# Kernel tuning notes

Measured on AMD Instinct MI355X. Metric: run time of the kernel, lower is better.

## Reference

```python
import jax, jax.numpy as jnp
import numpy as np


def _bilinear_resample(inputs, offsets):
    # inputs: (b, s, s, c); offsets: (b, s, s, 2) -- faithful to tf_batch_map_offsets
    b, h, w, c = inputs.shape
    s = h  # square map assumed by original code (input_size = shape[1])
    n = h * w
    offs = offsets.reshape(b, n, 2)
    gi, gj = jnp.meshgrid(jnp.arange(s, dtype=inputs.dtype),
                          jnp.arange(s, dtype=inputs.dtype), indexing='ij')
    grid = jnp.stack([gi, gj], axis=-1).reshape(1, n, 2)
    coords = jnp.clip(offs + grid, 0.0, float(s - 1))  # (b, n, 2), [i, j]
    lt = jnp.floor(coords).astype(jnp.int32)  # (b, n, 2)
    rb = jnp.ceil(coords).astype(jnp.int32)
    bidx = jnp.arange(b)[:, None]  # (b, 1) broadcasts with (b, n) index maps

    def gather(ci, cj):
        return inputs[bidx, ci, cj]  # (b, n, c)

    vals_lt = gather(lt[..., 0], lt[..., 1])
    vals_rb = gather(rb[..., 0], rb[..., 1])
    vals_lb = gather(rb[..., 0], lt[..., 1])  # [ceil_i, floor_j]
    vals_rt = gather(lt[..., 0], rb[..., 1])  # [floor_i, ceil_j]

    frac = coords - lt.astype(coords.dtype)  # (b, n, 2) fractional offsets
    fy = frac[..., 1:2]  # column fraction (axis 1 of coords)
    fx = frac[..., 0:1]  # row fraction
    vals_t = vals_lt + (vals_rt - vals_lt) * fy
    vals_b = vals_lb + (vals_rb - vals_lb) * fy
    out = vals_t + (vals_b - vals_t) * fx  # (b, n, c)
    return out.reshape(b, h, w, c)


def setup_inputs() -> dict:
    key = jax.random.key(0)
    k1, k2 = jax.random.split(key)
    B, S, C = 16, 128, 128
    offsets = jax.random.normal(k1, (B, S, S, 2), dtype=jnp.float32)
    inputs = jax.random.normal(k2, (B, S, S, C), dtype=jnp.float32)
    return {"offsets": offsets, "inputs": inputs}


def reference(offsets, inputs):
    return _bilinear_resample(inputs, offsets)
```

## Files before the change

### kernel.cpp

```cpp
#include <hip/hip_runtime.h>


constexpr int S = 128;
constexpr int CVEC = 32;
constexpr int PIX_PER_BLOCK = 8;
constexpr int NXCD = 8;
constexpr int ROWS_PER_SLAB = S / NXCD;
constexpr int SEGS = S / PIX_PER_BLOCK;

typedef float vf4 __attribute__((ext_vector_type(4)));

__global__ __launch_bounds__(256) void resample_kernel(
    const float* __restrict__ offsets,
    const vf4*  __restrict__ inputs4,
    vf4*        __restrict__ out4)
{
    const int tid     = threadIdx.x;
    const int lane_c  = tid & 31;
    const int pix_blk = tid >> 5;

    const int x   = blockIdx.x;
    const int xcd = x & (NXCD - 1);
    const int g   = x >> 3;
    const int r   = g & (ROWS_PER_SLAB - 1);
    const int seg = (g >> 4) & (SEGS - 1);
    const int b   = g >> 8;

    const int i = xcd * ROWS_PER_SLAB + r;
    const int j = seg * PIX_PER_BLOCK + pix_blk;
    const int pix = (b * S + i) * S + j;

    const float oy = offsets[pix * 2 + 0];
    const float ox = offsets[pix * 2 + 1];
    float y = fminf(fmaxf((float)i + oy, 0.0f), (float)(S - 1));
    float xx = fminf(fmaxf((float)j + ox, 0.0f), (float)(S - 1));

    const float y0f = floorf(y);
    const float x0f = floorf(xx);
    const int y0 = (int)y0f;
    const int x0 = (int)x0f;
    const int y1 = (int)ceilf(y);
    const int x1 = (int)ceilf(xx);
    const float fy = y - y0f;
    const float fx = xx - x0f;

    const int base = (b * S * S) * CVEC + lane_c;
    const int r0 = base + y0 * (S * CVEC);
    const int r1 = base + y1 * (S * CVEC);

    const vf4 v00 = inputs4[r0 + x0 * CVEC];
    const vf4 v01 = inputs4[r0 + x1 * CVEC];
    const vf4 v10 = inputs4[r1 + x0 * CVEC];
    const vf4 v11 = inputs4[r1 + x1 * CVEC];

    const vf4 vt = v00 + (v01 - v00) * fx;
    const vf4 vb = v10 + (v11 - v10) * fx;
    const vf4 o  = vt + (vb - vt) * fy;

    __builtin_nontemporal_store(o, &out4[(long long)pix * CVEC + lane_c]);
}

extern "C" void kernel_launch(void* const* d_in, const int* in_sizes, int n_in,
                              void* d_out, int out_size, void* d_ws, size_t ws_size,
                              hipStream_t stream) {
    const float* offsets = (const float*)d_in[0];
    const vf4*   inputs4 = (const vf4*)d_in[1];
    vf4*         out4    = (vf4*)d_out;

    const int B = in_sizes[0] / (S * S * 2);
    const int total_pix = B * S * S;
    const int blocks = total_pix / PIX_PER_BLOCK;

    resample_kernel<<<blocks, 256, 0, stream>>>(offsets, inputs4, out4);
}
```

Baseline: 232.6 us.

## Process two pixels per thread and drop XCD-aware block swizzle

Each thread now handles two pixels (16 per block) and issues eight independent gather loads, which raises memory-level parallelism per thread and halves the block count. The XCD-slab block remapping is removed in favor of a linear pixel order, so neighboring blocks may now land on different XCDs and lose L2 locality for the shared input rows. More registers per thread may lower occupancy.

New measurement: 233.0 us. About the same (+0.2%).

```diff
diff --git a/kernel.cpp b/kernel.cpp
--- a/kernel.cpp
+++ b/kernel.cpp
@@ -3,10 +3,8 @@
 
 constexpr int S = 128;
 constexpr int CVEC = 32;
-constexpr int PIX_PER_BLOCK = 8;
-constexpr int NXCD = 8;
-constexpr int ROWS_PER_SLAB = S / NXCD;
-constexpr int SEGS = S / PIX_PER_BLOCK;
+constexpr int PIX_PER_BLOCK = 16;
+constexpr int HALF = 8;
 
 typedef float vf4 __attribute__((ext_vector_type(4)));
 
@@ -19,45 +17,59 @@
     const int lane_c  = tid & 31;
     const int pix_blk = tid >> 5;
 
-    const int x   = blockIdx.x;
-    const int xcd = x & (NXCD - 1);
-    const int g   = x >> 3;
-    const int r   = g & (ROWS_PER_SLAB - 1);
-    const int seg = (g >> 4) & (SEGS - 1);
-    const int b   = g >> 8;
+    const int pix0 = blockIdx.x * PIX_PER_BLOCK + pix_blk;
+    const int pix1 = pix0 + HALF;
 
-    const int i = xcd * ROWS_PER_SLAB + r;
-    const int j = seg * PIX_PER_BLOCK + pix_blk;
-    const int pix = (b * S + i) * S + j;
+    const int j0  = pix0 & (S - 1);
+    const int j1  = pix1 & (S - 1);
+    const int rem = pix0 >> 7;
+    const int i   = rem & (S - 1);
+    const int b   = rem >> 7;
 
-    const float oy = offsets[pix * 2 + 0];
-    const float ox = offsets[pix * 2 + 1];
-    float y = fminf(fmaxf((float)i + oy, 0.0f), (float)(S - 1));
-    float xx = fminf(fmaxf((float)j + ox, 0.0f), (float)(S - 1));
+    const float oy0 = offsets[pix0 * 2 + 0];
+    const float ox0 = offsets[pix0 * 2 + 1];
+    const float oy1 = offsets[pix1 * 2 + 0];
+    const float ox1 = offsets[pix1 * 2 + 1];
 
-    const float y0f = floorf(y);
-    const float x0f = floorf(xx);
-    const int y0 = (int)y0f;
-    const int x0 = (int)x0f;
-    const int y1 = (int)ceilf(y);
-    const int x1 = (int)ceilf(xx);
-    const float fy = y - y0f;
-    const float fx = xx - x0f;
+    const float fS1 = (float)(S - 1);
+    float y0c = fminf(fmaxf((float)i  + oy0, 0.0f), fS1);
+    float x0c = fminf(fmaxf((float)j0 + ox0, 0.0f), fS1);
+    float y1c = fminf(fmaxf((float)i  + oy1, 0.0f), fS1);
+    float x1c = fminf(fmaxf((float)j1 + ox1, 0.0f), fS1);
+
+    const float y0f = floorf(y0c), x0f = floorf(x0c);
+    const float y1f = floorf(y1c), x1f = floorf(x1c);
+    const int ay0 = (int)y0f, ax0 = (int)x0f;
+    const int ay1 = (int)ceilf(y0c), ax1 = (int)ceilf(x0c);
+    const int by0 = (int)y1f, bx0 = (int)x1f;
+    const int by1 = (int)ceilf(y1c), bx1 = (int)ceilf(x1c);
+    const float afy = y0c - y0f, afx = x0c - x0f;
+    const float bfy = y1c - y1f, bfx = x1c - x1f;
 
     const int base = (b * S * S) * CVEC + lane_c;
-    const int r0 = base + y0 * (S * CVEC);
-    const int r1 = base + y1 * (S * CVEC);
+    const int ar0 = base + ay0 * (S * CVEC);
+    const int ar1 = base + ay1 * (S * CVEC);
+    const int br0 = base + by0 * (S * CVEC);
+    const int br1 = base + by1 * (S * CVEC);
 
-    const vf4 v00 = inputs4[r0 + x0 * CVEC];
-    const vf4 v01 = inputs4[r0 + x1 * CVEC];
-    const vf4 v10 = inputs4[r1 + x0 * CVEC];
-    const vf4 v11 = inputs4[r1 + x1 * CVEC];
+    const vf4 a00 = inputs4[ar0 + ax0 * CVEC];
+    const vf4 a01 = inputs4[ar0 + ax1 * CVEC];
+    const vf4 a10 = inputs4[ar1 + ax0 * CVEC];
+    const vf4 a11 = inputs4[ar1 + ax1 * CVEC];
+    const vf4 b00 = inputs4[br0 + bx0 * CVEC];
+    const vf4 b01 = inputs4[br0 + bx1 * CVEC];
+    const vf4 b10 = inputs4[br1 + bx0 * CVEC];
+    const vf4 b11 = inputs4[br1 + bx1 * CVEC];
 
-    const vf4 vt = v00 + (v01 - v00) * fx;
-    const vf4 vb = v10 + (v11 - v10) * fx;
-    const vf4 o  = vt + (vb - vt) * fy;
+    const vf4 at = a00 + (a01 - a00) * afx;
+    const vf4 ab = a10 + (a11 - a10) * afx;
+    const vf4 ao = at + (ab - at) * afy;
+    const vf4 bt = b00 + (b01 - b00) * bfx;
+    const vf4 bb = b10 + (b11 - b10) * bfx;
+    const vf4 bo = bt + (bb - bt) * bfy;
 
-    __builtin_nontemporal_store(o, &out4[(long long)pix * CVEC + lane_c]);
+    __builtin_nontemporal_store(ao, &out4[(long long)pix0 * CVEC + lane_c]);
+    __builtin_nontemporal_store(bo, &out4[(long long)pix1 * CVEC + lane_c]);
 }
 
 extern "C" void kernel_launch(void* const* d_in, const int* in_sizes, int n_in,
```
